# Performance work log

Hardware: AMD Instinct MI355X
Metric: run time of the kernel (lower is better)

Reference implementation:

```python
import jax, jax.numpy as jnp
import numpy as np

S = 16384          # vision tokens (one image, 128x128 patches)
HID = 1280         # vision_hidden_size
H = 16             # num heads
D = HID // H       # head_dim = 80
L = 8              # vision_depth
FF = 3456          # vision_intermediate_size
WIN = 64           # tokens per attention window
UNIT = 4           # spatial_merge_size ** 2
OUT = 2048         # vision_out_hidden_size
PV = 3 * 2 * 16 * 16  # patch volume = 1536


def setup_inputs() -> dict:
    keys = iter(jax.random.split(jax.random.key(0), 32))
    def nrm(shape, fan_in):
        return jax.random.normal(next(keys), shape, jnp.float32) * (fan_in ** -0.5)
    ang = jax.random.uniform(next(keys), (S, D // 2), jnp.float32, 0.0, 2.0 * float(np.pi))
    ang = jnp.concatenate([ang, ang], axis=-1)  # rotate_half-compatible duplicated layout
    return {
        "x": jax.random.normal(next(keys), (S, PV), jnp.float32),
        "cos": jnp.cos(ang), "sin": jnp.sin(ang),
        "cu_seqlens": jnp.arange(S // WIN + 1, dtype=jnp.int32) * WIN,
        "pe_w": nrm((PV, HID), PV), "pe_b": jnp.zeros((HID,), jnp.float32),
        "ln1_w": jnp.ones((L, HID), jnp.float32), "ln1_b": jnp.zeros((L, HID), jnp.float32),
        "qkv_w": nrm((L, HID, 3 * HID), HID), "qkv_b": jnp.zeros((L, 3 * HID), jnp.float32),
        "proj_w": nrm((L, HID, HID), HID), "proj_b": jnp.zeros((L, HID), jnp.float32),
        "ln2_w": jnp.ones((L, HID), jnp.float32), "ln2_b": jnp.zeros((L, HID), jnp.float32),
        "fc1_w": nrm((L, HID, FF), HID), "fc1_b": jnp.zeros((L, FF), jnp.float32),
        "fc2_w": nrm((L, FF, HID), FF), "fc2_b": jnp.zeros((L, HID), jnp.float32),
        "m_ln_w": jnp.ones((HID,), jnp.float32), "m_ln_b": jnp.zeros((HID,), jnp.float32),
        "m_fc1_w": nrm((UNIT * HID, UNIT * HID), UNIT * HID), "m_fc1_b": jnp.zeros((UNIT * HID,), jnp.float32),
        "m_fc2_w": nrm((UNIT * HID, OUT), UNIT * HID), "m_fc2_b": jnp.zeros((OUT,), jnp.float32),
    }


def _ln(t, w, b, eps=1e-6):
    m = jnp.mean(t, axis=-1, keepdims=True)
    v = jnp.mean((t - m) ** 2, axis=-1, keepdims=True)
    return (t - m) * jax.lax.rsqrt(v + eps) * w + b


def _forward(cu_seqlens, x, cos, sin, pe_w, pe_b, ln1_w, ln1_b, qkv_w, qkv_b,
             proj_w, proj_b, ln2_w, ln2_b, fc1_w, fc1_b, fc2_w, fc2_b,
             m_ln_w, m_ln_b, m_fc1_w, m_fc1_b, m_fc2_w, m_fc2_b):
    NW = cu_seqlens.shape[0] - 1  # uniform windows (static)
    W = S // NW
    scale = D ** -0.5
    cosr = cos[:, None, :]  # [S,1,D]
    sinr = sin[:, None, :]

    def rope(t):  # t: [S,H,D]
        t1, t2 = jnp.split(t, 2, axis=-1)
        return t * cosr + jnp.concatenate((-t2, t1), axis=-1) * sinr

    h = x @ pe_w + pe_b  # patch embed: [S, HID]

    def block(h, p):
        l1w, l1b, qw, qb, pw, pb, l2w, l2b, f1w, f1b, f2w, f2b = p
        xn = _ln(h, l1w, l1b)
        q, k, v = jnp.split(xn @ qw + qb, 3, axis=-1)
        q = rope(q.reshape(S, H, D))
        k = rope(k.reshape(S, H, D))
        v = v.reshape(S, H, D)
        # block-diagonal (windowed) attention, fp32 scores as in source
        qw_ = q.reshape(NW, W, H, D)
        kw_ = k.reshape(NW, W, H, D)
        vw_ = v.reshape(NW, W, H, D)
        scores = jnp.einsum('wqhd,wkhd->whqk', qw_, kw_) * scale
        attn = jnp.einsum('whqk,wkhd->wqhd', jax.nn.softmax(scores, axis=-1), vw_)
        h = h + (attn.reshape(S, HID) @ pw + pb)
        xn2 = _ln(h, l2w, l2b)
        h = h + (jax.nn.gelu(xn2 @ f1w + f1b, approximate=True) @ f2w + f2b)
        return h, None

    h, _ = jax.lax.scan(block, h, (ln1_w, ln1_b, qkv_w, qkv_b, proj_w, proj_b,
                                   ln2_w, ln2_b, fc1_w, fc1_b, fc2_w, fc2_b))
    # patch merger (pre-shuffle norm)
    hm = _ln(h, m_ln_w, m_ln_b).reshape(-1, UNIT * HID)  # [S/4, 5120]
    return jax.nn.gelu(hm @ m_fc1_w + m_fc1_b, approximate=True) @ m_fc2_w + m_fc2_b


def reference(x, cos, sin, cu_seqlens, pe_w, pe_b, ln1_w, ln1_b, qkv_w, qkv_b,
              proj_w, proj_b, ln2_w, ln2_b, fc1_w, fc1_b, fc2_w, fc2_b,
              m_ln_w, m_ln_b, m_fc1_w, m_fc1_b, m_fc2_w, m_fc2_b):
    return _forward(cu_seqlens, x, cos, sin, pe_w, pe_b, ln1_w, ln1_b, qkv_w, qkv_b,
                    proj_w, proj_b, ln2_w, ln2_b, fc1_w, fc1_b, fc2_w, fc2_b,
                    m_ln_w, m_ln_b, m_fc1_w, m_fc1_b, m_fc2_w, m_fc2_b)
```

## Files before the change

kernel.cpp:

```cpp
#include <hip/hip_runtime.h>

typedef unsigned short ushortT;
typedef __attribute__((ext_vector_type(8))) short short8;
typedef __attribute__((ext_vector_type(8))) unsigned short ushort8;
typedef __attribute__((ext_vector_type(4))) unsigned short ushort4v;
typedef __attribute__((ext_vector_type(4))) float f32x4;

#define DEVINL __device__ __forceinline__

DEVINL ushortT f2bf(float f) {
    unsigned u = __builtin_bit_cast(unsigned, f);
    u += 0x7FFFu + ((u >> 16) & 1u);
    return (ushortT)(u >> 16);
}
DEVINL float bf2f(ushortT h) {
    unsigned u = ((unsigned)h) << 16;
    return __builtin_bit_cast(float, u);
}
DEVINL float gelu_tanh(float x) {
    float x3 = x * x * x;
    return 0.5f * x * (1.0f + tanhf(0.7978845608028654f * (x + 0.044715f * x3)));
}

#define GLOAD_LDS16(g, l)                                                     \
    __builtin_amdgcn_global_load_lds(                                         \
        (const __attribute__((address_space(1))) void*)(g),                   \
        (__attribute__((address_space(3))) void*)(l), 16, 0, 0)

#define WAITV(n) asm volatile("s_waitcnt vmcnt(" #n ")" ::: "memory")
#define MEMFENCE() asm volatile("" ::: "memory")
#define BAR() __builtin_amdgcn_s_barrier()
#define BARF() MEMFENCE(); BAR(); MEMFENCE()

__global__ __launch_bounds__(256) void cast_bf16_4(const float* __restrict__ in,
                                                   ushortT* __restrict__ out, long n4) {
    long i = (long)blockIdx.x * 256 + threadIdx.x;
    if (i < n4) {
        const float* p = in + i * 4;
        ushort4v o;
        o[0] = f2bf(p[0]); o[1] = f2bf(p[1]); o[2] = f2bf(p[2]); o[3] = f2bf(p[3]);
        ((ushort4v*)out)[i] = o;
    }
}

__global__ __launch_bounds__(256) void transpose_cast(const float* __restrict__ in,
                                                      ushortT* __restrict__ out,
                                                      int K, int N, int Npad) {
    __shared__ float tile[32][33];
    long zi = (long)blockIdx.z * K * N;
    long zo = (long)blockIdx.z * Npad * K;
    const float* ip = in + zi;
    ushortT* op = out + zo;
    int t = threadIdx.x, bx = blockIdx.x, by = blockIdx.y;
#pragma unroll
    for (int i = 0; i < 4; i++) {
        int idx = i * 256 + t, r = idx >> 5, c = idx & 31;
        int col = bx * 32 + c;
        tile[r][c] = (col < N) ? ip[(long)(by * 32 + r) * N + col] : 0.0f;
    }
    __syncthreads();
#pragma unroll
    for (int i = 0; i < 4; i++) {
        int idx = i * 256 + t, r = idx >> 5, c = idx & 31;
        op[(long)(bx * 32 + r) * K + by * 32 + c] = f2bf(tile[c][r]);
    }
}

__global__ __launch_bounds__(256) void pad_bias(const float* __restrict__ in,
                                                float* __restrict__ out,
                                                int n_in, int n_out, int total) {
    int i = blockIdx.x * 256 + threadIdx.x;
    if (i < total) {
        int l = i / n_out, c = i % n_out;
        out[i] = (c < n_in) ? in[l * n_in + c] : 0.0f;
    }
}

__global__ __launch_bounds__(256) void ln_bf16(const ushortT* __restrict__ in,
                                               const float* __restrict__ w,
                                               const float* __restrict__ b,
                                               ushortT* __restrict__ out) {
    const int row = blockIdx.x;
    const ushortT* x = in + (long)row * 1280;
    __shared__ float red[4];
    const int t = threadIdx.x;
    float v[8];
    float s = 0.f;
    if (t < 160) {
        ushort8 u = *(const ushort8*)(x + t * 8);
#pragma unroll
        for (int i = 0; i < 8; i++) { v[i] = bf2f(u[i]); s += v[i]; }
    } else {
#pragma unroll
        for (int i = 0; i < 8; i++) v[i] = 0.f;
    }
#pragma unroll
    for (int o = 32; o > 0; o >>= 1) s += __shfl_xor(s, o);
    int wave = t >> 6;
    if ((t & 63) == 0) red[wave] = s;
    __syncthreads();
    float mean = (red[0] + red[1] + red[2] + red[3]) * (1.0f / 1280.0f);
    float q = 0.f;
    if (t < 160) {
#pragma unroll
        for (int i = 0; i < 8; i++) { float d = v[i] - mean; q += d * d; }
    }
#pragma unroll
    for (int o = 32; o > 0; o >>= 1) q += __shfl_xor(q, o);
    __syncthreads();
    if ((t & 63) == 0) red[wave] = q;
    __syncthreads();
    float var = (red[0] + red[1] + red[2] + red[3]) * (1.0f / 1280.0f);
    float rs = rsqrtf(var + 1e-6f);
    if (t < 160) {
        ushort8 o8;
#pragma unroll
        for (int i = 0; i < 8; i++) {
            int c = t * 8 + i;
            o8[i] = f2bf((v[i] - mean) * rs * w[c] + b[c]);
        }
        *(ushort8*)(out + (long)row * 1280 + t * 8) = o8;
    }
}


#define WSTAGE_A(k0, buf)                                                     \
    _Pragma("unroll") for (int j = 0; j < 4; j++) {                           \
        int c = j * 256 + t; int sr = c >> 2, sl = c & 3;                     \
        GLOAD_LDS16(A + (brow + sr) * (size_t)lda + (k0) + ((sl ^ ((sr >> 1) & 3)) * 8), \
                    &lsA[buf][c * 8]);                                        \
    }
#define WSTAGE_B(k0, buf)                                                     \
    _Pragma("unroll") for (int j = 0; j < 2; j++) {                           \
        int c = j * 256 + t; int sr = c >> 2, sl = c & 3;                     \
        GLOAD_LDS16(Bt + (bcol + sr) * (size_t)ldb + (k0) + ((sl ^ ((sr >> 1) & 3)) * 8), \
                    &lsB[buf][c * 8]);                                        \
    }
#define WREAD(buf)                                                            \
    _Pragma("unroll") for (int m = 0; m < 8; m++) {                           \
        int r = wr * 128 + m * 16 + lr;                                       \
        aF[m] = *(const short8*)&lsA[buf][r * 32 + ((lg ^ ((r >> 1) & 3)) * 8)]; \
    }                                                                         \
    _Pragma("unroll") for (int n = 0; n < 4; n++) {                           \
        int r = wc * 64 + n * 16 + lr;                                        \
        bF[n] = *(const short8*)&lsB[buf][r * 32 + ((lg ^ ((r >> 1) & 3)) * 8)]; \
    }
#define WMFMA()                                                               \
    __builtin_amdgcn_s_setprio(1);                                            \
    _Pragma("unroll") for (int m = 0; m < 8; m++)                             \
    _Pragma("unroll") for (int n = 0; n < 4; n++)                             \
        acc[m][n] = __builtin_amdgcn_mfma_f32_16x16x32_bf16(                  \
            aF[m], bF[n], acc[m][n], 0, 0, 0);                                \
    __builtin_amdgcn_s_setprio(0);

template <bool OBF, bool RESB, bool GEL>
__global__ __launch_bounds__(256, 2)
void gemm_wide(const ushortT* __restrict__ A, const ushortT* __restrict__ Bt,
               const float* __restrict__ bias, const ushortT* __restrict__ resb,
               void* __restrict__ out, int M, int N, int K, int lda, int ldb) {
    __shared__ ushortT lsA[2][8192];
    __shared__ ushortT lsB[2][4096];
    const int t = threadIdx.x;
    const int lane = t & 63, lr = lane & 15, lg = lane >> 4;
    const int wave = t >> 6;
    const int wr = wave >> 1, wc = wave & 1;

    const int nwg = gridDim.x, orig = blockIdx.x;
    const int q = nwg >> 3, r8 = nwg & 7;
    const int xcd = orig & 7, loc = orig >> 3;
    const int wg = (xcd < r8 ? xcd * (q + 1) : r8 * (q + 1) + (xcd - r8) * q) + loc;
    const int gx = N >> 7;
    const size_t brow = (size_t)(wg / gx) * 256;
    const size_t bcol = (size_t)(wg % gx) * 128;

    f32x4 acc[8][4];
#pragma unroll
    for (int m = 0; m < 8; m++)
#pragma unroll
        for (int n = 0; n < 4; n++) acc[m][n] = f32x4{0.f, 0.f, 0.f, 0.f};

    WSTAGE_A(0, 0);
    WSTAGE_B(0, 0);
    WAITV(0); BARF();

    short8 aF[8], bF[4];
    const int NT = K >> 5;
    int cur = 0;
    for (int tt = 0; tt < NT; ++tt) {
        MEMFENCE();
        WREAD(cur);
        if (tt + 1 < NT) {
            const int k1 = (tt + 1) << 5;
            WSTAGE_A(k1, cur ^ 1);
            WSTAGE_B(k1, cur ^ 1);
        }
        WMFMA();
        if (tt + 1 < NT) {
            WAITV(0);
            BARF();
        }
        cur ^= 1;
    }

#pragma unroll
    for (int m = 0; m < 8; m++) {
#pragma unroll
        for (int n = 0; n < 4; n++) {
#pragma unroll
            for (int rr = 0; rr < 4; rr++) {
                size_t row = brow + wr * 128 + m * 16 + lg * 4 + rr;
                size_t col = bcol + wc * 64 + n * 16 + lr;
                float v = acc[m][n][rr] + bias[col];
                if (RESB) v += bf2f(resb[row * N + col]);
                if (GEL) v = gelu_tanh(v);
                if (OBF) ((ushortT*)out)[row * N + col] = f2bf(v);
                else     ((float*)out)[row * N + col] = v;
            }
        }
    }
}

__global__ __launch_bounds__(256) void attn_win(const ushortT* __restrict__ qkv,
                                                const float* __restrict__ cosb,
                                                const float* __restrict__ sinb,
                                                ushortT* __restrict__ out) {
    const int w = blockIdx.x, h = blockIdx.y;
    __shared__ ushortT qs[64 * 96];
    __shared__ ushortT ks[64 * 96];
    __shared__ ushortT vt[80 * 80];
    __shared__ float   sc[64 * 65];
    __shared__ ushortT pb[64 * 80];
    const int t = threadIdx.x, wave = t >> 6, lane = t & 63, lr = lane & 15, lg = lane >> 4;
    const ushortT* bq = qkv + (long)w * 64 * 3840 + h * 80;

    for (int c = t; c < 640; c += 256) {
        int r = c / 10, cb = c % 10;
        const ushortT* qp = bq + (long)r * 3840;
        ushort8 qa = *(const ushort8*)(qp + cb * 8);
        ushort8 ka = *(const ushort8*)(qp + 1280 + cb * 8);
        int pcb = (cb < 5) ? cb + 5 : cb - 5;
        ushort8 qpr = *(const ushort8*)(qp + pcb * 8);
        ushort8 kpr = *(const ushort8*)(qp + 1280 + pcb * 8);
        long srow = (long)w * 64 + r;
        const float* cp = cosb + srow * 80 + cb * 8;
        const float* sp = sinb + srow * 80 + cb * 8;
        float sgn = (cb < 5) ? -1.f : 1.f;
        ushort8 qo, ko;
#pragma unroll
        for (int j = 0; j < 8; j++) {
            float c_ = cp[j], s_ = sp[j] * sgn;
            qo[j] = f2bf(bf2f(qa[j]) * c_ + bf2f(qpr[j]) * s_);
            ko[j] = f2bf(bf2f(ka[j]) * c_ + bf2f(kpr[j]) * s_);
        }
        *(ushort8*)&qs[r * 96 + cb * 8] = qo;
        *(ushort8*)&ks[r * 96 + cb * 8] = ko;
        ushort8 vv = *(const ushort8*)(qp + 2560 + cb * 8);
#pragma unroll
        for (int j = 0; j < 8; j++) vt[(cb * 8 + j) * 80 + r] = vv[j];
    }
    for (int idx = t; idx < 1024; idx += 256) {
        int r = idx >> 4, c2 = 80 + (idx & 15);
        qs[r * 96 + c2] = 0;
        ks[r * 96 + c2] = 0;
    }
    __syncthreads();

    f32x4 sa[4];
#pragma unroll
    for (int n = 0; n < 4; n++) sa[n] = f32x4{0.f, 0.f, 0.f, 0.f};
#pragma unroll
    for (int kk = 0; kk < 3; kk++) {
        short8 aq = *(const short8*)&qs[(wave * 16 + lr) * 96 + kk * 32 + lg * 8];
#pragma unroll
        for (int n = 0; n < 4; n++) {
            short8 bk = *(const short8*)&ks[(n * 16 + lr) * 96 + kk * 32 + lg * 8];
            sa[n] = __builtin_amdgcn_mfma_f32_16x16x32_bf16(aq, bk, sa[n], 0, 0, 0);
        }
    }
    const float scale = 0.11180339887498949f;
#pragma unroll
    for (int n = 0; n < 4; n++)
#pragma unroll
        for (int r = 0; r < 4; r++)
            sc[(wave * 16 + lg * 4 + r) * 65 + n * 16 + lr] = sa[n][r] * scale;
    __syncthreads();

    {
        int row = t >> 2, q4 = t & 3;
        float pv[16];
        float mx = -1e30f;
#pragma unroll
        for (int j = 0; j < 16; j++) { pv[j] = sc[row * 65 + q4 * 16 + j]; mx = fmaxf(mx, pv[j]); }
        mx = fmaxf(mx, __shfl_xor(mx, 1));
        mx = fmaxf(mx, __shfl_xor(mx, 2));
        float sum = 0.f;
#pragma unroll
        for (int j = 0; j < 16; j++) { pv[j] = __expf(pv[j] - mx); sum += pv[j]; }
        sum += __shfl_xor(sum, 1);
        sum += __shfl_xor(sum, 2);
        float inv = 1.0f / sum;
#pragma unroll
        for (int j = 0; j < 16; j++) pb[row * 80 + q4 * 16 + j] = f2bf(pv[j] * inv);
    }
    __syncthreads();

    f32x4 pa[5];
#pragma unroll
    for (int n = 0; n < 5; n++) pa[n] = f32x4{0.f, 0.f, 0.f, 0.f};
#pragma unroll
    for (int kk = 0; kk < 2; kk++) {
        short8 ap = *(const short8*)&pb[(wave * 16 + lr) * 80 + kk * 32 + lg * 8];
#pragma unroll
        for (int n = 0; n < 5; n++) {
            short8 bv = *(const short8*)&vt[(n * 16 + lr) * 80 + kk * 32 + lg * 8];
            pa[n] = __builtin_amdgcn_mfma_f32_16x16x32_bf16(ap, bv, pa[n], 0, 0, 0);
        }
    }
    ushortT* ob = out + (long)w * 64 * 1280 + h * 80;
#pragma unroll
    for (int n = 0; n < 5; n++)
#pragma unroll
        for (int r = 0; r < 4; r++)
            ob[(long)(wave * 16 + lg * 4 + r) * 1280 + n * 16 + lr] = f2bf(pa[n][r]);
}

extern "C" void kernel_launch(void* const* d_in, const int* in_sizes, int n_in,
                              void* d_out, int out_size, void* d_ws, size_t ws_size,
                              hipStream_t stream) {
    const float* x      = (const float*)d_in[0];
    const float* cosb   = (const float*)d_in[1];
    const float* sinb   = (const float*)d_in[2];
    const float* pe_w   = (const float*)d_in[4];
    const float* pe_b   = (const float*)d_in[5];
    const float* ln1_w  = (const float*)d_in[6];
    const float* ln1_b  = (const float*)d_in[7];
    const float* qkv_w  = (const float*)d_in[8];
    const float* qkv_b  = (const float*)d_in[9];
    const float* proj_w = (const float*)d_in[10];
    const float* proj_b = (const float*)d_in[11];
    const float* ln2_w  = (const float*)d_in[12];
    const float* ln2_b  = (const float*)d_in[13];
    const float* fc1_w  = (const float*)d_in[14];
    const float* fc1_b  = (const float*)d_in[15];
    const float* fc2_w  = (const float*)d_in[16];
    const float* fc2_b  = (const float*)d_in[17];
    const float* mln_w  = (const float*)d_in[18];
    const float* mln_b  = (const float*)d_in[19];
    const float* mfc1_w = (const float*)d_in[20];
    const float* mfc1_b = (const float*)d_in[21];
    const float* mfc2_w = (const float*)d_in[22];
    const float* mfc2_b = (const float*)d_in[23];

    char* ws = (char*)d_ws;
    size_t off = 0;
    auto alloc = [&](size_t bytes) -> char* {
        char* p = ws + off;
        off += (bytes + 255) & ~(size_t)255;
        return p;
    };
    ushortT* pe_wT   = (ushortT*)alloc((size_t)1280 * 1536 * 2);
    ushortT* qkv_wT  = (ushortT*)alloc((size_t)8 * 3840 * 1280 * 2);
    ushortT* proj_wT = (ushortT*)alloc((size_t)8 * 1280 * 1280 * 2);
    ushortT* fc1_wT  = (ushortT*)alloc((size_t)8 * 3584 * 1280 * 2);
    ushortT* fc2_wT  = (ushortT*)alloc((size_t)8 * 1280 * 3456 * 2);
    ushortT* mfc1_wT = (ushortT*)alloc((size_t)5120 * 5120 * 2);
    ushortT* mfc2_wT = (ushortT*)alloc((size_t)2048 * 5120 * 2);
    float*   fc1_bp  = (float*)alloc((size_t)8 * 3584 * 4);
    ushortT* hbuf    = (ushortT*)alloc((size_t)16384 * 1280 * 2);
    ushortT* xn      = (ushortT*)alloc((size_t)16384 * 1280 * 2);
    ushortT* big     = (ushortT*)alloc((size_t)16384 * 3840 * 2);
    ushortT* attnb   = (ushortT*)alloc((size_t)16384 * 1280 * 2);

    ushortT* xbf  = big;
    ushortT* qkvb = big;
    ushortT* ffn1 = big;
    ushortT* t1   = attnb;

    transpose_cast<<<dim3(1280 / 32, 1536 / 32, 1), 256, 0, stream>>>(pe_w,   pe_wT,   1536, 1280, 1280);
    transpose_cast<<<dim3(3840 / 32, 1280 / 32, 8), 256, 0, stream>>>(qkv_w,  qkv_wT,  1280, 3840, 3840);
    transpose_cast<<<dim3(1280 / 32, 1280 / 32, 8), 256, 0, stream>>>(proj_w, proj_wT, 1280, 1280, 1280);
    transpose_cast<<<dim3(3584 / 32, 1280 / 32, 8), 256, 0, stream>>>(fc1_w,  fc1_wT,  1280, 3456, 3584);
    transpose_cast<<<dim3(1280 / 32, 3456 / 32, 8), 256, 0, stream>>>(fc2_w,  fc2_wT,  3456, 1280, 1280);
    transpose_cast<<<dim3(5120 / 32, 5120 / 32, 1), 256, 0, stream>>>(mfc1_w, mfc1_wT, 5120, 5120, 5120);
    transpose_cast<<<dim3(2048 / 32, 5120 / 32, 1), 256, 0, stream>>>(mfc2_w, mfc2_wT, 5120, 2048, 2048);
    pad_bias<<<(8 * 3584 + 255) / 256, 256, 0, stream>>>(fc1_b, fc1_bp, 3456, 3584, 8 * 3584);

    cast_bf16_4<<<(16384L * 1536 / 4 + 255) / 256, 256, 0, stream>>>(x, xbf, 16384L * 1536 / 4);
    gemm_wide<true, false, false><<<dim3(64 * 10), 256, 0, stream>>>(
        xbf, pe_wT, pe_b, nullptr, hbuf, 16384, 1280, 1536, 1536, 1536);

    for (int l = 0; l < 8; l++) {
        ln_bf16<<<16384, 256, 0, stream>>>(hbuf, ln1_w + l * 1280, ln1_b + l * 1280, xn);
        gemm_wide<true, false, false><<<dim3(64 * 30), 256, 0, stream>>>(
            xn, qkv_wT + (size_t)l * 3840 * 1280, qkv_b + l * 3840, nullptr, qkvb,
            16384, 3840, 1280, 1280, 1280);
        attn_win<<<dim3(256, 16), 256, 0, stream>>>(qkvb, cosb, sinb, attnb);
        gemm_wide<true, true, false><<<dim3(64 * 10), 256, 0, stream>>>(
            attnb, proj_wT + (size_t)l * 1280 * 1280, proj_b + l * 1280, hbuf, hbuf,
            16384, 1280, 1280, 1280, 1280);
        ln_bf16<<<16384, 256, 0, stream>>>(hbuf, ln2_w + l * 1280, ln2_b + l * 1280, xn);
        gemm_wide<true, false, true><<<dim3(64 * 28), 256, 0, stream>>>(
            xn, fc1_wT + (size_t)l * 3584 * 1280, fc1_bp + l * 3584, nullptr, ffn1,
            16384, 3584, 1280, 1280, 1280);
        gemm_wide<true, true, false><<<dim3(64 * 10), 256, 0, stream>>>(
            ffn1, fc2_wT + (size_t)l * 1280 * 3456, fc2_b + l * 1280, hbuf, hbuf,
            16384, 1280, 3456, 3584, 3456);
    }

    ln_bf16<<<16384, 256, 0, stream>>>(hbuf, mln_w, mln_b, xn);
    gemm_wide<true, false, true><<<dim3(16 * 40), 256, 0, stream>>>(
        xn, mfc1_wT, mfc1_b, nullptr, t1, 4096, 5120, 5120, 5120, 5120);
    gemm_wide<false, false, false><<<dim3(16 * 16), 256, 0, stream>>>(
        t1, mfc2_wT, mfc2_b, nullptr, (float*)d_out, 4096, 2048, 5120, 5120, 5120);
}
```

Measured before the change: 6.889 ms.

## Add 128x128 double-buffered GEMM for narrow-N layers to raise wave occupancy

Adds a new gemm_db kernel that uses 128x128 output tiles, double-buffered LDS staging, and XCD-aware workgroup remapping, with launch bounds of 2 blocks per CU. It replaces the wide-tile GEMM for the patch embed, proj, fc2 and merger fc2 layers, where N is only 1280 or 2048 and the old 256-row tiles gave few workgroups (640 or 256). The goal is better CU fill and tail behaviour on these narrow GEMMs. The cost is less A/B reuse per tile and more global loads, and the epilogue does scalar per-element stores.

Measured after the change: 6.723 ms (median of 2 runs). 1.02x faster.

```diff
diff --git a/kernel.cpp b/kernel.cpp
--- a/kernel.cpp
+++ b/kernel.cpp
@@ -123,6 +123,95 @@
     }
 }
 
+#define GSTAGE(mat, ls, base, ld, k0, buf)                                    \
+    _Pragma("unroll") for (int j = 0; j < 2; j++) {                           \
+        int c = j * 256 + t; int sr = c >> 2, sl = c & 3;                     \
+        GLOAD_LDS16(mat + (base + sr) * (size_t)ld + (k0) + ((sl ^ ((sr >> 1) & 3)) * 8), \
+                    &ls[buf][c * 8]);                                         \
+    }
+#define GREAD(buf)                                                            \
+    _Pragma("unroll") for (int m = 0; m < 4; m++) {                           \
+        int r = wr * 64 + m * 16 + lr;                                        \
+        aF[m] = *(const short8*)&lsA[buf][r * 32 + ((lg ^ ((r >> 1) & 3)) * 8)]; \
+    }                                                                         \
+    _Pragma("unroll") for (int n = 0; n < 4; n++) {                           \
+        int r = wc * 64 + n * 16 + lr;                                        \
+        bF[n] = *(const short8*)&lsB[buf][r * 32 + ((lg ^ ((r >> 1) & 3)) * 8)]; \
+    }
+#define GMFMA()                                                               \
+    __builtin_amdgcn_s_setprio(1);                                            \
+    _Pragma("unroll") for (int m = 0; m < 4; m++)                             \
+    _Pragma("unroll") for (int n = 0; n < 4; n++)                             \
+        acc[m][n] = __builtin_amdgcn_mfma_f32_16x16x32_bf16(                  \
+            aF[m], bF[n], acc[m][n], 0, 0, 0);                                \
+    __builtin_amdgcn_s_setprio(0);
+
+template <bool OBF, bool RESB, bool GEL>
+__global__ __launch_bounds__(256, 2)
+void gemm_db(const ushortT* __restrict__ A, const ushortT* __restrict__ Bt,
+             const float* __restrict__ bias, const ushortT* __restrict__ resb,
+             void* __restrict__ out, int M, int N, int K, int lda, int ldb) {
+    __shared__ ushortT lsA[2][4096];
+    __shared__ ushortT lsB[2][4096];
+    const int t = threadIdx.x;
+    const int lane = t & 63, lr = lane & 15, lg = lane >> 4;
+    const int wave = t >> 6;
+    const int wr = wave >> 1, wc = wave & 1;
+
+    const int nwg = gridDim.x, orig = blockIdx.x;
+    const int q = nwg >> 3, r8 = nwg & 7;
+    const int xcd = orig & 7, loc = orig >> 3;
+    const int wg = (xcd < r8 ? xcd * (q + 1) : r8 * (q + 1) + (xcd - r8) * q) + loc;
+    const int gx = N >> 7;
+    const size_t brow = (size_t)(wg / gx) * 128;
+    const size_t bcol = (size_t)(wg % gx) * 128;
+
+    f32x4 acc[4][4];
+#pragma unroll
+    for (int m = 0; m < 4; m++)
+#pragma unroll
+        for (int n = 0; n < 4; n++) acc[m][n] = f32x4{0.f, 0.f, 0.f, 0.f};
+
+    GSTAGE(A, lsA, brow, lda, 0, 0);
+    GSTAGE(Bt, lsB, bcol, ldb, 0, 0);
+    WAITV(0); BARF();
+
+    short8 aF[4], bF[4];
+    const int NT = K >> 5;
+    int cur = 0;
+    for (int tt = 0; tt < NT; ++tt) {
+        MEMFENCE();
+        GREAD(cur);
+        if (tt + 1 < NT) {
+            const int k1 = (tt + 1) << 5;
+            GSTAGE(A, lsA, brow, lda, k1, cur ^ 1);
+            GSTAGE(Bt, lsB, bcol, ldb, k1, cur ^ 1);
+        }
+        GMFMA();
+        if (tt + 1 < NT) {
+            WAITV(0);
+            BARF();
+        }
+        cur ^= 1;
+    }
+
+#pragma unroll
+    for (int m = 0; m < 4; m++) {
+#pragma unroll
+        for (int n = 0; n < 4; n++) {
+#pragma unroll
+            for (int rr = 0; rr < 4; rr++) {
+                size_t row = brow + wr * 64 + m * 16 + lg * 4 + rr;
+                size_t col = bcol + wc * 64 + n * 16 + lr;
+                float v = acc[m][n][rr] + bias[col];
+                if (RESB) v += bf2f(resb[row * N + col]);
+                if (GEL) v = gelu_tanh(v);
+                if (OBF) ((ushortT*)out)[row * N + col] = f2bf(v);
+                else     ((float*)out)[row * N + col] = v;
+            }
+        }
+    }
+}
 
 #define WSTAGE_A(k0, buf)                                                     \
     _Pragma("unroll") for (int j = 0; j < 4; j++) {                           \
@@ -386,7 +475,7 @@
     pad_bias<<<(8 * 3584 + 255) / 256, 256, 0, stream>>>(fc1_b, fc1_bp, 3456, 3584, 8 * 3584);
 
     cast_bf16_4<<<(16384L * 1536 / 4 + 255) / 256, 256, 0, stream>>>(x, xbf, 16384L * 1536 / 4);
-    gemm_wide<true, false, false><<<dim3(64 * 10), 256, 0, stream>>>(
+    gemm_db<true, false, false><<<dim3(128 * 10), 256, 0, stream>>>(
         xbf, pe_wT, pe_b, nullptr, hbuf, 16384, 1280, 1536, 1536, 1536);
 
     for (int l = 0; l < 8; l++) {
@@ -395,14 +484,14 @@
             xn, qkv_wT + (size_t)l * 3840 * 1280, qkv_b + l * 3840, nullptr, qkvb,
             16384, 3840, 1280, 1280, 1280);
         attn_win<<<dim3(256, 16), 256, 0, stream>>>(qkvb, cosb, sinb, attnb);
-        gemm_wide<true, true, false><<<dim3(64 * 10), 256, 0, stream>>>(
+        gemm_db<true, true, false><<<dim3(128 * 10), 256, 0, stream>>>(
             attnb, proj_wT + (size_t)l * 1280 * 1280, proj_b + l * 1280, hbuf, hbuf,
             16384, 1280, 1280, 1280, 1280);
         ln_bf16<<<16384, 256, 0, stream>>>(hbuf, ln2_w + l * 1280, ln2_b + l * 1280, xn);
         gemm_wide<true, false, true><<<dim3(64 * 28), 256, 0, stream>>>(
             xn, fc1_wT + (size_t)l * 3584 * 1280, fc1_bp + l * 3584, nullptr, ffn1,
             16384, 3584, 1280, 1280, 1280);
-        gemm_wide<true, true, false><<<dim3(64 * 10), 256, 0, stream>>>(
+        gemm_db<true, true, false><<<dim3(128 * 10), 256, 0, stream>>>(
             ffn1, fc2_wT + (size_t)l * 1280 * 3456, fc2_b + l * 1280, hbuf, hbuf,
             16384, 1280, 3456, 3584, 3456);
     }
@@ -410,6 +499,6 @@
     ln_bf16<<<16384, 256, 0, stream>>>(hbuf, mln_w, mln_b, xn);
     gemm_wide<true, false, true><<<dim3(16 * 40), 256, 0, stream>>>(
         xn, mfc1_wT, mfc1_b, nullptr, t1, 4096, 5120, 5120, 5120, 5120);
-    gemm_wide<false, false, false><<<dim3(16 * 16), 256, 0, stream>>>(
+    gemm_db<false, false, false><<<dim3(32 * 16), 256, 0, stream>>>(
         t1, mfc2_wT, mfc2_b, nullptr, (float*)d_out, 4096, 2048, 5120, 5120, 5120);
 }
```
